# Kernel optimization log

Hardware: AMD Instinct MI355X
Metric: run time of the kernel (lower is better)

## Reference

```python
import jax, jax.numpy as jnp
import numpy as np

EPS = 1e-5
N_GROUPS = 32
N_HEAD = 1


def group_norm(x, gamma, beta):
    B, C, H, W = x.shape
    xg = x.reshape(B, N_GROUPS, C // N_GROUPS, H, W)
    mean = xg.mean(axis=(2, 3, 4), keepdims=True)
    var = xg.var(axis=(2, 3, 4), keepdims=True)
    xg = (xg - mean) * jax.lax.rsqrt(var + EPS)
    x = xg.reshape(B, C, H, W)
    return x * gamma[None, :, None, None] + beta[None, :, None, None]


def setup_inputs() -> dict:
    key = jax.random.key(0)
    k1, k2, k3 = jax.random.split(key, 3)
    B, C, H, W = 32, 512, 32, 32
    x = jax.random.normal(k1, (B, C, H, W), dtype=jnp.float32)
    gamma = jnp.ones((C,), dtype=jnp.float32)
    beta = jnp.zeros((C,), dtype=jnp.float32)
    # fan_avg uniform init for 1x1 convs (bound = sqrt(3*scale/fan_avg))
    bound_qkv = np.sqrt(3.0 / ((C + 3 * C) / 2))
    w_qkv = jax.random.uniform(k2, (3 * C, C), dtype=jnp.float32,
                               minval=-bound_qkv, maxval=bound_qkv)
    b_qkv = jnp.zeros((3 * C,), dtype=jnp.float32)
    bound_out = np.sqrt(3.0 * 1e-10 / C)
    w_out = jax.random.uniform(k3, (C, C), dtype=jnp.float32,
                               minval=-bound_out, maxval=bound_out)
    b_out = jnp.zeros((C,), dtype=jnp.float32)
    return {"x": x, "gamma": gamma, "beta": beta,
            "w_qkv": w_qkv, "b_qkv": b_qkv, "w_out": w_out, "b_out": b_out}


def reference(x, gamma, beta, w_qkv, b_qkv, w_out, b_out):
    B, C, H, W = x.shape
    n_head = N_HEAD
    head_dim = C // n_head
    norm = group_norm(x, gamma, beta)
    # 1x1 conv == channel matmul: [B,3C,H,W]
    qkv = jnp.einsum('bchw,oc->bohw', norm, w_qkv) + b_qkv[None, :, None, None]
    qkv = qkv.reshape(B, n_head, 3 * head_dim, H, W)
    q, k, v = jnp.split(qkv, 3, axis=2)  # each [B,n,hd,H,W]
    scale = 1.0 / np.sqrt(head_dim)
    attn = jnp.einsum('bnchw,bncyx->bnhwyx', q, k) * scale
    attn = jax.nn.softmax(attn.reshape(B, n_head, H, W, H * W), axis=-1)
    attn = attn.reshape(B, n_head, H, W, H, W)
    out = jnp.einsum('bnhwyx,bncyx->bnchw', attn, v).reshape(B, C, H, W)
    out = jnp.einsum('bchw,oc->bohw', out, w_out) + b_out[None, :, None, None]
    return out + x
```

## Files before the change

kernel.cpp:

```cpp
#include <hip/hip_runtime.h>
#include <hip/hip_bf16.h>

#define B_    32
#define C_    512
#define S_    1024
#define G_    32
#define CPG_  16
#define EPS_  1e-5f
#define SCALE_ 0.044194173824159216f
#define ZS_    1024.0f
#define VS_    1048576.0f
#define INVZS_ 0.0009765625f
#define INVVS_ 9.5367431640625e-07f

typedef __attribute__((ext_vector_type(4))) float  floatx4;
typedef __attribute__((ext_vector_type(8))) __bf16 bf16x8;
typedef long lng;

__device__ __forceinline__ float bf2f(unsigned short u) {
    union { unsigned int i; float f; } v; v.i = ((unsigned int)u) << 16; return v.f;
}
__device__ __forceinline__ unsigned short f2bf(float f) {
    union { float f; unsigned int i; } v; v.f = f;
    unsigned int r = v.i + 0x7fffu + ((v.i >> 16) & 1u);
    return (unsigned short)(r >> 16);
}
__device__ __forceinline__ unsigned int f2f8x4(float a, float b, float c, float d) {
    unsigned int v = (unsigned int)__builtin_amdgcn_cvt_pk_fp8_f32(a, b, 0, false);
    v = (unsigned int)__builtin_amdgcn_cvt_pk_fp8_f32(c, d, (int)v, true);
    return v;
}

__device__ __forceinline__ void gl16(const void* g, void* l) {
    __builtin_amdgcn_global_load_lds(
        (const __attribute__((address_space(1))) unsigned int*)g,
        (__attribute__((address_space(3))) unsigned int*)l, 16, 0, 0);
}

__global__ __launch_bounds__(256) void gnxnt(const float* __restrict__ x,
                                             const float* __restrict__ gamma,
                                             const float* __restrict__ beta,
                                             unsigned char* __restrict__ xnt,
                                             float* __restrict__ lbuf) {
    const int bid = blockIdx.x;
    const int b = bid >> 5, g = bid & 31;
    if (threadIdx.x < 8)
        ((float4*)lbuf)[bid * 8 + threadIdx.x] = make_float4(0.f, 0.f, 0.f, 0.f);

    __shared__ float tile[16 * 1025];
    __shared__ float a1[4], a2[4];
    const float* xb = x + (size_t)b * (C_ * S_) + (size_t)g * (CPG_ * S_);
    const int t = threadIdx.x;

    float s = 0.f, ss = 0.f;
    #pragma unroll
    for (int k = 0; k < 16; k++) {
        int idx = t + k * 256;
        float4 v = ((const float4*)xb)[idx];
        int c = idx >> 8, s4 = (idx & 255) * 4;
        float* dst = tile + c * 1025 + s4;
        dst[0] = v.x; dst[1] = v.y; dst[2] = v.z; dst[3] = v.w;
        s  += v.x + v.y + v.z + v.w;
        ss += v.x * v.x + v.y * v.y + v.z * v.z + v.w * v.w;
    }
    #pragma unroll
    for (int o = 32; o; o >>= 1) { s += __shfl_down(s, o); ss += __shfl_down(ss, o); }
    const int wid = t >> 6, lane = t & 63;
    if (lane == 0) { a1[wid] = s; a2[wid] = ss; }
    __syncthreads();
    float S  = a1[0] + a1[1] + a1[2] + a1[3];
    float SS = a2[0] + a2[1] + a2[2] + a2[3];
    float mean = S * (1.f / 16384.f);
    float var  = SS * (1.f / 16384.f) - mean * mean;
    float rstd = rsqrtf(var + EPS_);

    const int c0 = g * 16, cc = (t & 3) * 4;
    float av[4], bv[4];
    #pragma unroll
    for (int i = 0; i < 4; i++) {
        float a_ = rstd * gamma[c0 + cc + i];
        av[i] = a_; bv[i] = beta[c0 + cc + i] - mean * a_;
    }
    unsigned char* xo = xnt + (size_t)b * (S_ * C_) + c0 + cc;
    #pragma unroll
    for (int p = 0; p < 16; p++) {
        int srow = p * 64 + (t >> 2);
        const float* col = tile + srow;
        unsigned int o4 = f2f8x4(av[0] * col[(cc + 0) * 1025] + bv[0],
                                 av[1] * col[(cc + 1) * 1025] + bv[1],
                                 av[2] * col[(cc + 2) * 1025] + bv[2],
                                 av[3] * col[(cc + 3) * 1025] + bv[3]);
        *(unsigned int*)(xo + (size_t)srow * C_) = o4;
    }
}

__global__ __launch_bounds__(256) void tcast(const float* __restrict__ w,
                                             const float* __restrict__ w_out,
                                             unsigned short* __restrict__ WqT,
                                             unsigned short* __restrict__ WkT,
                                             unsigned short* __restrict__ WvT,
                                             unsigned short* __restrict__ Woutb) {
    const int z = blockIdx.z;
    const int m0 = blockIdx.y * 64, c0 = blockIdx.x * 64;
    const int t = threadIdx.x, tr = t >> 4, tc4 = (t & 15) * 4;
    if (z == 3) {
        #pragma unroll
        for (int i = 0; i < 4; i++) {
            int r = tr + i * 16;
            float4 v = *(const float4*)(w_out + (size_t)(m0 + r) * 512 + c0 + tc4);
            ushort4 o4;
            o4.x = f2bf(v.x); o4.y = f2bf(v.y); o4.z = f2bf(v.z); o4.w = f2bf(v.w);
            *(ushort4*)(Woutb + (size_t)(m0 + r) * 512 + c0 + tc4) = o4;
        }
        return;
    }
    const float* src = w + (size_t)z * 262144;
    unsigned short* dst = (z == 0) ? WqT : (z == 1) ? WkT : WvT;
    __shared__ float tile[64][65];
    #pragma unroll
    for (int i = 0; i < 4; i++) {
        int r = tr + i * 16;
        float4 v = *(const float4*)(src + (size_t)(m0 + r) * 512 + c0 + tc4);
        tile[r][tc4 + 0] = v.x; tile[r][tc4 + 1] = v.y;
        tile[r][tc4 + 2] = v.z; tile[r][tc4 + 3] = v.w;
    }
    __syncthreads();
    #pragma unroll
    for (int i = 0; i < 4; i++) {
        int sr = tr + i * 16;
        ushort4 o4;
        o4.x = f2bf(tile[tc4 + 0][sr]); o4.y = f2bf(tile[tc4 + 1][sr]);
        o4.z = f2bf(tile[tc4 + 2][sr]); o4.w = f2bf(tile[tc4 + 3][sr]);
        *(ushort4*)(dst + (size_t)(c0 + sr) * 512 + m0 + tc4) = o4;
    }
}

__global__ __launch_bounds__(256) void vecprep(const unsigned short* __restrict__ WkT,
                                               const float* __restrict__ w_out,
                                               const float* __restrict__ b_qkv,
                                               float* __restrict__ bzv) {
    const int o = blockIdx.x, t = threadIdx.x;
    float us = 0.f, bv = 0.f;
    #pragma unroll
    for (int mm = 0; mm < 2; mm++) {
        int m = t + mm * 256;
        us += b_qkv[m] * bf2f(WkT[(size_t)o * 512 + m]);
        bv += w_out[(size_t)o * 512 + m] * b_qkv[1024 + m];
    }
    #pragma unroll
    for (int sh = 32; sh; sh >>= 1) { us += __shfl_down(us, sh); bv += __shfl_down(bv, sh); }
    __shared__ float a[2][4];
    const int wid = t >> 6, lane = t & 63;
    if (lane == 0) { a[0][wid] = us; a[1][wid] = bv; }
    __syncthreads();
    if (t == 0) {
        bzv[o]       = (a[0][0] + a[0][1] + a[0][2] + a[0][3]) * SCALE_ * ZS_;
        bzv[512 + o] = (a[1][0] + a[1][1] + a[1][2] + a[1][3]) * VS_;
    }
}

template<bool SWAP>
__device__ __forceinline__ void mfma_loop(const unsigned short* __restrict__ Ag, int lda,
                                          const unsigned short* __restrict__ Bg, int ldb,
                                          int K, int m0, int n0,
                                          unsigned short* ldsA, unsigned short* ldsB,
                                          floatx4 (&acc)[4][4]) {
    const int t = threadIdx.x, lane = t & 63, wave = t >> 6;
    const int wr = (wave >> 1) * 64, wc = (wave & 1) * 64;
    const int lrow = lane & 15, lq = lane >> 4;
    const int srow = wave * 16 + (lane >> 2);
    const int scol = (lane & 3) * 8;
    const unsigned short* gA0 = Ag + (size_t)(m0 + srow) * lda + scol;
    const unsigned short* gA1 = gA0 + (size_t)64 * lda;
    const unsigned short* gB0 = Bg + (size_t)(n0 + srow) * ldb + scol;
    const unsigned short* gB1 = gB0 + (size_t)64 * ldb;
    unsigned short* lA = ldsA + wave * 512;
    unsigned short* lB = ldsB + wave * 512;
    for (int k0 = 0; k0 < K; k0 += 64) {
        gl16(gA0 + k0,      lA);
        gl16(gA1 + k0,      lA + 2048);
        gl16(gA0 + k0 + 32, lA + 4096);
        gl16(gA1 + k0 + 32, lA + 6144);
        gl16(gB0 + k0,      lB);
        gl16(gB1 + k0,      lB + 2048);
        gl16(gB0 + k0 + 32, lB + 4096);
        gl16(gB1 + k0 + 32, lB + 6144);
        __syncthreads();
        #pragma unroll
        for (int sub = 0; sub < 2; sub++) {
            bf16x8 af[4], bfr[4];
            #pragma unroll
            for (int i = 0; i < 4; i++) {
                af[i]  = *(const bf16x8*)(ldsA + sub * 4096 + (wr + i * 16 + lrow) * 32 + lq * 8);
                bfr[i] = *(const bf16x8*)(ldsB + sub * 4096 + (wc + i * 16 + lrow) * 32 + lq * 8);
            }
            #pragma unroll
            for (int i = 0; i < 4; i++)
                #pragma unroll
                for (int j = 0; j < 4; j++) {
                    if (SWAP)
                        acc[i][j] = __builtin_amdgcn_mfma_f32_16x16x32_bf16(bfr[j], af[i], acc[i][j], 0, 0, 0);
                    else
                        acc[i][j] = __builtin_amdgcn_mfma_f32_16x16x32_bf16(af[i], bfr[j], acc[i][j], 0, 0, 0);
                }
        }
        __syncthreads();
    }
}

__global__ __launch_bounds__(256) void prep_gemm(const unsigned short* __restrict__ WkT,
                                                 const unsigned short* __restrict__ WqT,
                                                 const unsigned short* __restrict__ Woutb,
                                                 const unsigned short* __restrict__ WvT,
                                                 unsigned char* __restrict__ Wzv) {
    __shared__ __align__(16) unsigned short ldsA[2 * 128 * 32];
    __shared__ __align__(16) unsigned short ldsB[2 * 128 * 32];
    const int z = blockIdx.z;
    const int m0 = blockIdx.y * 128, n0 = blockIdx.x * 128;
    const int t = threadIdx.x, lane = t & 63, wave = t >> 6;
    const int wr = (wave >> 1) * 64, wc = (wave & 1) * 64;
    const int lrow = lane & 15, lq = lane >> 4;
    floatx4 acc[4][4];
    #pragma unroll
    for (int i = 0; i < 4; i++)
        #pragma unroll
        for (int j = 0; j < 4; j++) acc[i][j] = (floatx4){0.f, 0.f, 0.f, 0.f};
    const unsigned short* Ag = z ? Woutb : WkT;
    const unsigned short* Bg = z ? WvT   : WqT;
    mfma_loop<true>(Ag, 512, Bg, 512, 512, m0, n0, ldsA, ldsB, acc);
    const float sc = z ? VS_ : (SCALE_ * ZS_);
    #pragma unroll
    for (int i = 0; i < 4; i++)
        #pragma unroll
        for (int j = 0; j < 4; j++) {
            int row = z * 512 + m0 + wr + i * 16 + lrow;
            int col = n0 + wc + j * 16 + lq * 4;
            floatx4 v = acc[i][j];
            unsigned int o4 = f2f8x4(v[0] * sc, v[1] * sc, v[2] * sc, v[3] * sc);
            *(unsigned int*)(Wzv + (size_t)row * 512 + col) = o4;
        }
}

template<bool SWAP>
__device__ __forceinline__ void mfma256f8_loop(const unsigned char* __restrict__ Ag, int lda,
                                               const unsigned char* __restrict__ Bg, int ldb,
                                               int nt, int m0, int n0,
                                               unsigned char* lds, floatx4 (&acc)[8][4]) {
    const int tid  = threadIdx.x;
    const int lane = tid & 63, wave = tid >> 6;
    const int wm = wave >> 2, wn = wave & 3;
    const int lrow = lane & 15, lq = lane >> 4;
    const int swz  = (lrow >> 1) & 3;
    const int hb   = (lq & 1) * 8;
    const int slb  = lq >> 1;
    const int s0 = ((slb    ) ^ swz) * 16 + hb;
    const int s1 = ((slb + 2) ^ swz) * 16 + hb;

    int aof[8], bof[4];
    #pragma unroll
    for (int i = 0; i < 8; i++) aof[i] = (wm * 128 + i * 16 + lrow) * 64;
    #pragma unroll
    for (int j = 0; j < 4; j++) bof[j] = 65536 + (wn * 64 + j * 16 + lrow) * 64;

    const int sr  = tid >> 2;
    const int scs = (tid & 3) ^ ((tid >> 3) & 3);
    const unsigned char* gA = Ag + (size_t)(m0 + sr) * lda + scs * 16;
    const unsigned char* gB = Bg + (size_t)(n0 + sr) * ldb + scs * 16;
    const size_t a128 = (size_t)128 * lda, b128 = (size_t)128 * ldb;
    unsigned char* lwA = lds + wave * 1024;
    unsigned char* lwB = lds + 65536 + wave * 1024;

#define STAGE_A(t, kh) do { \
    unsigned char* lb_ = lwA + ((t) & 1) * 32768 + (kh) * 16384; \
    const unsigned char* gp_ = gA + (t) * 128 + (kh) * 64; \
    gl16(gp_, lb_); gl16(gp_ + a128, lb_ + 8192); } while (0)
#define STAGE_B(t, kh) do { \
    unsigned char* lb_ = lwB + ((t) & 1) * 32768 + (kh) * 16384; \
    const unsigned char* gp_ = gB + (t) * 128 + (kh) * 64; \
    gl16(gp_, lb_); gl16(gp_ + b128, lb_ + 8192); } while (0)

    STAGE_A(0, 0); STAGE_B(0, 0); STAGE_A(0, 1); STAGE_B(0, 1);
    STAGE_A(1, 0); STAGE_B(1, 0);
    asm volatile("s_waitcnt vmcnt(4)" ::: "memory");
    __builtin_amdgcn_s_barrier();

    lng af0[4], af1[4], bf0[4], bf1[4];
    for (int u = 0; u < nt; ++u) {
        const int p = u & 1;
        #pragma unroll
        for (int ph = 0; ph < 4; ++ph) {
            const int kh = ph >> 1, mh = ph & 1;
            const int slab = p * 32768 + kh * 16384;
            if (mh == 0) {
                #pragma unroll
                for (int j = 0; j < 4; j++) {
                    bf0[j] = *(const lng*)(lds + slab + bof[j] + s0);
                    bf1[j] = *(const lng*)(lds + slab + bof[j] + s1);
                }
            }
            #pragma unroll
            for (int i = 0; i < 4; i++) {
                af0[i] = *(const lng*)(lds + slab + aof[mh * 4 + i] + s0);
                af1[i] = *(const lng*)(lds + slab + aof[mh * 4 + i] + s1);
            }
            if (ph == 0)      { if (u + 1 < nt) STAGE_A(u + 1, 1); }
            else if (ph == 1) { if (u + 1 < nt) STAGE_B(u + 1, 1); }
            else if (ph == 2) { if (u + 2 < nt) STAGE_A(u + 2, 0); }
            else              { if (u + 2 < nt) STAGE_B(u + 2, 0); }
            __builtin_amdgcn_s_barrier();
            asm volatile("s_waitcnt lgkmcnt(0)" ::: "memory");
            __builtin_amdgcn_sched_barrier(0);
            __builtin_amdgcn_s_setprio(1);
            #pragma unroll
            for (int i = 0; i < 4; i++)
                #pragma unroll
                for (int j = 0; j < 4; j++) {
                    if (SWAP)
                        acc[mh * 4 + i][j] = __builtin_amdgcn_mfma_f32_16x16x32_fp8_fp8(
                            bf0[j], af0[i], acc[mh * 4 + i][j], 0, 0, 0);
                    else
                        acc[mh * 4 + i][j] = __builtin_amdgcn_mfma_f32_16x16x32_fp8_fp8(
                            af0[i], bf0[j], acc[mh * 4 + i][j], 0, 0, 0);
                }
            #pragma unroll
            for (int i = 0; i < 4; i++)
                #pragma unroll
                for (int j = 0; j < 4; j++) {
                    if (SWAP)
                        acc[mh * 4 + i][j] = __builtin_amdgcn_mfma_f32_16x16x32_fp8_fp8(
                            bf1[j], af1[i], acc[mh * 4 + i][j], 0, 0, 0);
                    else
                        acc[mh * 4 + i][j] = __builtin_amdgcn_mfma_f32_16x16x32_fp8_fp8(
                            af1[i], bf1[j], acc[mh * 4 + i][j], 0, 0, 0);
                }
            __builtin_amdgcn_s_setprio(0);
            if (ph < 3) {
                __builtin_amdgcn_s_barrier();
            } else if (u < nt - 2) {
                asm volatile("s_waitcnt vmcnt(4)" ::: "memory");
                __builtin_amdgcn_s_barrier();
            } else if (u == nt - 2) {
                asm volatile("s_waitcnt vmcnt(0)" ::: "memory");
                __builtin_amdgcn_s_barrier();
            }
        }
    }
#undef STAGE_A
#undef STAGE_B
}

#define GEMMF8_VARS                                                   \
    __shared__ __align__(16) unsigned char lds[131072];               \
    const int lane = threadIdx.x & 63, wave = threadIdx.x >> 6;       \
    const int wm = wave >> 2, wn = wave & 3;                          \
    const int lrow = lane & 15, lq = lane >> 4;                       \
    floatx4 acc[8][4];                                                \
    _Pragma("unroll") for (int i = 0; i < 8; i++)                     \
        _Pragma("unroll") for (int j = 0; j < 4; j++)                 \
            acc[i][j] = (floatx4){0.f, 0.f, 0.f, 0.f};

__global__ __launch_bounds__(512, 2) void zv_mfma(const unsigned char* __restrict__ Wzv,
                                                  const unsigned char* __restrict__ xnt,
                                                  const float* __restrict__ bzv,
                                                  unsigned char* __restrict__ Zb,
                                                  unsigned char* __restrict__ Vb) {
    const int f = blockIdx.x;
    const int xcd = f & 7, j = f >> 3;
    const int b = xcd + 8 * (j >> 4);
    const int tile = j & 15;
    const int m0 = (tile >> 2) * 256, n0 = (tile & 3) * 256;
    GEMMF8_VARS
    const unsigned char* Bg = xnt + (size_t)b * (S_ * C_);
    if (m0 < 512) {
        mfma256f8_loop<false>(Wzv, C_, Bg, C_, 4, m0, n0, lds, acc);
        unsigned char* dst = Zb + (size_t)b * (S_ * C_);
        #pragma unroll
        for (int i = 0; i < 8; i++)
            #pragma unroll
            for (int j2 = 0; j2 < 4; j2++) {
                int oabs = m0 + wm * 128 + i * 16 + lq * 4;
                int s    = n0 + wn * 64 + j2 * 16 + lrow;
                float4 bi = *(const float4*)(bzv + oabs);
                floatx4 v = acc[i][j2];
                unsigned int o4 = f2f8x4(v[0] + bi.x, v[1] + bi.y,
                                         v[2] + bi.z, v[3] + bi.w);
                *(unsigned int*)(dst + (size_t)s * C_ + oabs) = o4;
            }
    } else {
        mfma256f8_loop<true>(Wzv, C_, Bg, C_, 4, m0, n0, lds, acc);
        unsigned char* dst = Vb + (size_t)b * (C_ * S_);
        #pragma unroll
        for (int i = 0; i < 8; i++)
            #pragma unroll
            for (int j2 = 0; j2 < 4; j2++) {
                int row = m0 + wm * 128 + i * 16 + lrow;
                int c   = row - 512;
                int sb  = n0 + wn * 64 + j2 * 16 + lq * 4;
                float bi = bzv[row];
                floatx4 v = acc[i][j2];
                unsigned int o4 = f2f8x4(v[0] + bi, v[1] + bi, v[2] + bi, v[3] + bi);
                *(unsigned int*)(dst + (size_t)c * S_ + sb) = o4;
            }
    }
}

__global__ __launch_bounds__(512, 2) void scores_exp(const unsigned char* __restrict__ Zb,
                                                     const unsigned char* __restrict__ xnt,
                                                     unsigned char* __restrict__ Pb,
                                                     float* __restrict__ l) {
    const int f = blockIdx.x;
    const int xcd = f & 7, j = f >> 3;
    const int b = xcd + 8 * (j >> 4);
    const int tile = j & 15;
    const int m0 = (tile >> 2) * 256, n0 = (tile & 3) * 256;
    GEMMF8_VARS
    const unsigned char* Ag = Zb  + (size_t)b * (S_ * C_);
    const unsigned char* Bg = xnt + (size_t)b * (S_ * C_);
    mfma256f8_loop<true>(Ag, C_, Bg, C_, 4, m0, n0, lds, acc);
    unsigned char* pp = Pb + (size_t)b * ((size_t)S_ * S_);
    float* lb = l + b * S_;
    float rsv[8];
    #pragma unroll
    for (int i = 0; i < 8; i++) {
        int q = m0 + wm * 128 + i * 16 + lrow;
        float rs = 0.f;
        #pragma unroll
        for (int j2 = 0; j2 < 4; j2++) {
            int kv = n0 + wn * 64 + j2 * 16 + lq * 4;
            floatx4 v = acc[i][j2];
            float e0 = __expf(v[0] * INVZS_), e1 = __expf(v[1] * INVZS_);
            float e2 = __expf(v[2] * INVZS_), e3 = __expf(v[3] * INVZS_);
            rs += (e0 + e1) + (e2 + e3);
            *(unsigned int*)(pp + (size_t)q * S_ + kv) = f2f8x4(e0, e1, e2, e3);
        }
        rs += __shfl_xor(rs, 16);
        rs += __shfl_xor(rs, 32);
        rsv[i] = rs;
    }
    __syncthreads();
    float* sred = (float*)lds;
    if (lane < 16) {
        #pragma unroll
        for (int i = 0; i < 8; i++)
            sred[wn * 256 + wm * 128 + i * 16 + lrow] = rsv[i];
    }
    __syncthreads();
    if (threadIdx.x < 256) {
        int q = threadIdx.x;
        float sum = (sred[q] + sred[256 + q]) + (sred[512 + q] + sred[768 + q]);
        atomicAdd(lb + m0 + q, sum);
    }
}

__global__ __launch_bounds__(512, 2) void pv_out(const unsigned char* __restrict__ Vb,
                                                 const unsigned char* __restrict__ Pb,
                                                 const float* __restrict__ l,
                                                 const float* __restrict__ bout,
                                                 const float* __restrict__ x,
                                                 float* __restrict__ out) {
    const int f = blockIdx.x;
    const int xcd = f & 7, j = f >> 3;
    const int b = xcd + 8 * (j >> 3);
    const int tile = j & 7;
    const int m0 = (tile & 1) * 256, n0 = (tile >> 1) * 256;
    GEMMF8_VARS
    const unsigned char* Ag = Vb + (size_t)b * (C_ * S_);
    const unsigned char* Bg = Pb + (size_t)b * ((size_t)S_ * S_);
    mfma256f8_loop<true>(Ag, S_, Bg, S_, 8, m0, n0, lds, acc);
    const float* lb = l + b * S_;
    const float* xb = x + (size_t)b * (C_ * S_);
    float* ob = out + (size_t)b * (C_ * S_);
    #pragma unroll
    for (int i = 0; i < 8; i++) {
        int c = m0 + wm * 128 + i * 16 + lrow;
        float bb = bout[c];
        #pragma unroll
        for (int j2 = 0; j2 < 4; j2++) {
            int s = n0 + wn * 64 + j2 * 16 + lq * 4;
            float4 lv = *(const float4*)(lb + s);
            size_t idx = (size_t)c * S_ + s;
            float4 xv = *(const float4*)(xb + idx);
            floatx4 v = acc[i][j2];
            float4 r;
            r.x = v[0] * (__frcp_rn(lv.x) * INVVS_) + bb + xv.x;
            r.y = v[1] * (__frcp_rn(lv.y) * INVVS_) + bb + xv.y;
            r.z = v[2] * (__frcp_rn(lv.z) * INVVS_) + bb + xv.z;
            r.w = v[3] * (__frcp_rn(lv.w) * INVVS_) + bb + xv.w;
            *(float4*)(ob + idx) = r;
        }
    }
}

extern "C" void kernel_launch(void* const* d_in, const int* in_sizes, int n_in,
                              void* d_out, int out_size, void* d_ws, size_t ws_size,
                              hipStream_t stream) {
    const float* x      = (const float*)d_in[0];
    const float* gamma  = (const float*)d_in[1];
    const float* beta   = (const float*)d_in[2];
    const float* w_qkv  = (const float*)d_in[3];
    const float* b_qkv  = (const float*)d_in[4];
    const float* w_out  = (const float*)d_in[5];
    const float* b_out  = (const float*)d_in[6];
    float* out          = (float*)d_out;

    char* ws = (char*)d_ws;
    unsigned char* Zb    = (unsigned char*)(ws);
    unsigned char* Vb    = (unsigned char*)(ws + 16777216ULL);
    unsigned char* xnt   = (unsigned char*)(ws + 33554432ULL);
    unsigned char* Pb    = (unsigned char*)(ws + 50331648ULL);
    unsigned short* WqT   = (unsigned short*)(ws + 100663296ULL);
    unsigned short* WkT   = (unsigned short*)(ws + 100663296ULL + 524288ULL);
    unsigned short* WvT   = (unsigned short*)(ws + 100663296ULL + 1048576ULL);
    unsigned short* Woutb = (unsigned short*)(ws + 100663296ULL + 1572864ULL);
    unsigned char*  Wzv   = (unsigned char*)(ws + 100663296ULL + 2097152ULL);
    float*          bzv   = (float*)(ws + 100663296ULL + 2621440ULL);
    float*          lbuf  = (float*)(ws + 100663296ULL + 2629632ULL);

    gnxnt    <<<B_ * G_, 256, 0, stream>>>(x, gamma, beta, xnt, lbuf);
    tcast    <<<dim3(8, 8, 4), 256, 0, stream>>>(w_qkv, w_out, WqT, WkT, WvT, Woutb);
    prep_gemm<<<dim3(4, 4, 2), 256, 0, stream>>>(WkT, WqT, Woutb, WvT, Wzv);
    vecprep  <<<512, 256, 0, stream>>>(WkT, w_out, b_qkv, bzv);
    zv_mfma  <<<512, 512, 0, stream>>>(Wzv, xnt, bzv, Zb, Vb);
    scores_exp<<<512, 512, 0, stream>>>(Zb, xnt, Pb, lbuf);
    pv_out   <<<256, 512, 0, stream>>>(Vb, Pb, lbuf, b_out, x, out);
}
```

Measured before the change: 286.3 us.

## Restructure FP8 GEMM main loop into two k-half phases with one-tile prefetch

The FP8 MFMA GEMM main loop drops from four phases per tile (k-half × m-half) to two k-half phases, each loading all eight A fragments and running 64 MFMAs. The global-to-LDS prefetch now runs one tile ahead instead of two, and A and B halves are staged together in each phase. This cuts the number of block barriers per tile and gives each barrier a longer MFMA run to cover. In exchange it holds more fragment registers, which could hurt occupancy, and leaves less time to hide global-load latency.

```diff
diff --git a/kernel.cpp b/kernel.cpp
--- a/kernel.cpp
+++ b/kernel.cpp
@@ -280,66 +280,57 @@
     gl16(gp_, lb_); gl16(gp_ + b128, lb_ + 8192); } while (0)
 
     STAGE_A(0, 0); STAGE_B(0, 0); STAGE_A(0, 1); STAGE_B(0, 1);
-    STAGE_A(1, 0); STAGE_B(1, 0);
     asm volatile("s_waitcnt vmcnt(4)" ::: "memory");
     __builtin_amdgcn_s_barrier();
 
-    lng af0[4], af1[4], bf0[4], bf1[4];
+    lng af0[8], af1[8], bf0[4], bf1[4];
     for (int u = 0; u < nt; ++u) {
         const int p = u & 1;
         #pragma unroll
-        for (int ph = 0; ph < 4; ++ph) {
-            const int kh = ph >> 1, mh = ph & 1;
+        for (int kh = 0; kh < 2; ++kh) {
             const int slab = p * 32768 + kh * 16384;
-            if (mh == 0) {
-                #pragma unroll
-                for (int j = 0; j < 4; j++) {
-                    bf0[j] = *(const lng*)(lds + slab + bof[j] + s0);
-                    bf1[j] = *(const lng*)(lds + slab + bof[j] + s1);
-                }
+            #pragma unroll
+            for (int j = 0; j < 4; j++) {
+                bf0[j] = *(const lng*)(lds + slab + bof[j] + s0);
+                bf1[j] = *(const lng*)(lds + slab + bof[j] + s1);
             }
             #pragma unroll
-            for (int i = 0; i < 4; i++) {
-                af0[i] = *(const lng*)(lds + slab + aof[mh * 4 + i] + s0);
-                af1[i] = *(const lng*)(lds + slab + aof[mh * 4 + i] + s1);
+            for (int i = 0; i < 8; i++) {
+                af0[i] = *(const lng*)(lds + slab + aof[i] + s0);
+                af1[i] = *(const lng*)(lds + slab + aof[i] + s1);
             }
-            if (ph == 0)      { if (u + 1 < nt) STAGE_A(u + 1, 1); }
-            else if (ph == 1) { if (u + 1 < nt) STAGE_B(u + 1, 1); }
-            else if (ph == 2) { if (u + 2 < nt) STAGE_A(u + 2, 0); }
-            else              { if (u + 2 < nt) STAGE_B(u + 2, 0); }
+            if (u + 1 < nt) { STAGE_A(u + 1, kh); STAGE_B(u + 1, kh); }
             __builtin_amdgcn_s_barrier();
             asm volatile("s_waitcnt lgkmcnt(0)" ::: "memory");
             __builtin_amdgcn_sched_barrier(0);
             __builtin_amdgcn_s_setprio(1);
             #pragma unroll
-            for (int i = 0; i < 4; i++)
+            for (int i = 0; i < 8; i++)
                 #pragma unroll
                 for (int j = 0; j < 4; j++) {
                     if (SWAP)
-                        acc[mh * 4 + i][j] = __builtin_amdgcn_mfma_f32_16x16x32_fp8_fp8(
-                            bf0[j], af0[i], acc[mh * 4 + i][j], 0, 0, 0);
+                        acc[i][j] = __builtin_amdgcn_mfma_f32_16x16x32_fp8_fp8(
+                            bf0[j], af0[i], acc[i][j], 0, 0, 0);
                     else
-                        acc[mh * 4 + i][j] = __builtin_amdgcn_mfma_f32_16x16x32_fp8_fp8(
-                            af0[i], bf0[j], acc[mh * 4 + i][j], 0, 0, 0);
+                        acc[i][j] = __builtin_amdgcn_mfma_f32_16x16x32_fp8_fp8(
+                            af0[i], bf0[j], acc[i][j], 0, 0, 0);
                 }
             #pragma unroll
-            for (int i = 0; i < 4; i++)
+            for (int i = 0; i < 8; i++)
                 #pragma unroll
                 for (int j = 0; j < 4; j++) {
                     if (SWAP)
-                        acc[mh * 4 + i][j] = __builtin_amdgcn_mfma_f32_16x16x32_fp8_fp8(
-                            bf1[j], af1[i], acc[mh * 4 + i][j], 0, 0, 0);
+                        acc[i][j] = __builtin_amdgcn_mfma_f32_16x16x32_fp8_fp8(
+                            bf1[j], af1[i], acc[i][j], 0, 0, 0);
                     else
-                        acc[mh * 4 + i][j] = __builtin_amdgcn_mfma_f32_16x16x32_fp8_fp8(
-                            af1[i], bf1[j], acc[mh * 4 + i][j], 0, 0, 0);
+                        acc[i][j] = __builtin_amdgcn_mfma_f32_16x16x32_fp8_fp8(
+                            af1[i], bf1[j], acc[i][j], 0, 0, 0);
                 }
             __builtin_amdgcn_s_setprio(0);
-            if (ph < 3) {
-                __builtin_amdgcn_s_barrier();
-            } else if (u < nt - 2) {
+            if (u < nt - 1) {
                 asm volatile("s_waitcnt vmcnt(4)" ::: "memory");
                 __builtin_amdgcn_s_barrier();
-            } else if (u == nt - 2) {
+            } else if (kh == 0) {
                 asm volatile("s_waitcnt vmcnt(0)" ::: "memory");
                 __builtin_amdgcn_s_barrier();
             }
```

Measured after the change: 286.6 us. About the same (+0.1%).
